# Kernel tuning notes

Hardware: AMD Instinct MI355X
Metric: run time of the kernel (lower is better)

The kernel has to match this reference:

```python
import jax, jax.numpy as jnp
import numpy as np

B, S, HID, LAYERS, HEADS, WINDOW = 2, 4096, 768, 4, 12, 256
W = WINDOW // 2            # one-sided window: each token attends to W left, W right
HD = HID // HEADS          # head dim = 64
MAXPOS = (S // WINDOW + 1) * WINDOW + 1
EPS = 1e-12                # Longformer layer_norm_eps


def layer_norm(x, g, b):
    m = x.mean(-1, keepdims=True)
    v = ((x - m) ** 2).mean(-1, keepdims=True)
    return (x - m) * jax.lax.rsqrt(v + EPS) * g + b


def sliding_window_attention(q, k, v, key_mask):
    # q,k,v: [B,H,S,D]; key_mask: [B,S] bool. Band attention: |i-j| <= W.
    Bz, Hh, Sl, D = q.shape
    nC = Sl // W
    q = q / jnp.sqrt(jnp.asarray(D, q.dtype))
    cidx = jnp.arange(nC)[:, None] + jnp.arange(3)[None, :]            # [nC,3] chunk gather
    kp = jnp.pad(k, ((0, 0), (0, 0), (W, W), (0, 0))).reshape(Bz, Hh, nC + 2, W, D)
    vp = jnp.pad(v, ((0, 0), (0, 0), (W, W), (0, 0))).reshape(Bz, Hh, nC + 2, W, D)
    kw = kp[:, :, cidx].reshape(Bz, Hh, nC, 3 * W, D)                  # keys for each query chunk
    vw = vp[:, :, cidx].reshape(Bz, Hh, nC, 3 * W, D)
    qc = q.reshape(Bz, Hh, nC, W, D)
    scores = jnp.einsum('bhcqd,bhckd->bhcqk', qc, kw)                  # [B,H,nC,W,3W]
    p = jnp.arange(W)[:, None]
    j = jnp.arange(3 * W)[None, :]
    band = (j >= p) & (j <= p + 2 * W)                                  # [W,3W] banded validity
    keypos = jnp.arange(nC)[:, None, None] * W + j[None] - W           # [nC,1,3W] global key idx
    inrange = (keypos >= 0) & (keypos < Sl)
    kmw = jnp.pad(key_mask, ((0, 0), (W, W))).reshape(Bz, nC + 2, W)[:, cidx].reshape(Bz, nC, 3 * W)
    mask = (band[None] & inrange)[None, None] & kmw[:, None, :, None, :]
    scores = jnp.where(mask, scores, jnp.asarray(-1e9, scores.dtype))
    probs = jax.nn.softmax(scores, axis=-1)
    out = jnp.einsum('bhcqk,bhckd->bhcqd', probs, vw)
    return out.reshape(Bz, Hh, Sl, D)


def heads_split(x):
    return x.reshape(x.shape[0], x.shape[1], HEADS, HD).transpose(0, 2, 1, 3)


def heads_merge(x):
    return x.transpose(0, 2, 1, 3).reshape(x.shape[0], x.shape[2], HID)


def forward(embeddings, pos_emb, tok_emb, emb_ln_g, emb_ln_b, Wq, bq, Wk, bk, Wv, bv,
            Wo, bo, ln1_g, ln1_b, Wi, bi, Wf, bf, ln2_g, ln2_b, Wp, bp, attention_mask):
    Sl = embeddings.shape[1]
    # Longformer embeddings: inputs_embeds + absolute positions (padding_idx+1 .. ) + token type 0
    h = embeddings + pos_emb[1:Sl + 1][None] + tok_emb[0][None, None]
    h = layer_norm(h, emb_ln_g, emb_ln_b)
    km = attention_mask.astype(bool)
    for l in range(LAYERS):
        q = heads_split(h @ Wq[l] + bq[l])
        k = heads_split(h @ Wk[l] + bk[l])
        v = heads_split(h @ Wv[l] + bv[l])
        a = heads_merge(sliding_window_attention(q, k, v, km))
        h = layer_norm(h + (a @ Wo[l] + bo[l]), ln1_g[l], ln1_b[l])
        f = jax.nn.gelu(h @ Wi[l] + bi[l], approximate=False) @ Wf[l] + bf[l]
        h = layer_norm(h + f, ln2_g[l], ln2_b[l])
    return jax.nn.sigmoid((h @ Wp + bp).squeeze(-1))


def setup_inputs() -> dict:
    key = jax.random.key(0)
    ks = jax.random.split(key, 12)
    nrm = lambda k, sh: jax.random.normal(k, sh, jnp.float32) * 0.02
    return dict(
        embeddings=jax.random.normal(ks[0], (B, S, HID), jnp.float32),
        attention_mask=jnp.ones((B, S), jnp.int32),
        pos_emb=nrm(ks[1], (MAXPOS, HID)),
        tok_emb=nrm(ks[2], (2, HID)),
        emb_ln_g=jnp.ones((HID,), jnp.float32),
        emb_ln_b=jnp.zeros((HID,), jnp.float32),
        Wq=nrm(ks[3], (LAYERS, HID, HID)), bq=jnp.zeros((LAYERS, HID), jnp.float32),
        Wk=nrm(ks[4], (LAYERS, HID, HID)), bk=jnp.zeros((LAYERS, HID), jnp.float32),
        Wv=nrm(ks[5], (LAYERS, HID, HID)), bv=jnp.zeros((LAYERS, HID), jnp.float32),
        Wo=nrm(ks[6], (LAYERS, HID, HID)), bo=jnp.zeros((LAYERS, HID), jnp.float32),
        ln1_g=jnp.ones((LAYERS, HID), jnp.float32), ln1_b=jnp.zeros((LAYERS, HID), jnp.float32),
        Wi=nrm(ks[7], (LAYERS, HID, 4 * HID)), bi=jnp.zeros((LAYERS, 4 * HID), jnp.float32),
        Wf=nrm(ks[8], (LAYERS, 4 * HID, HID)), bf=jnp.zeros((LAYERS, HID), jnp.float32),
        ln2_g=jnp.ones((LAYERS, HID), jnp.float32), ln2_b=jnp.zeros((LAYERS, HID), jnp.float32),
        Wp=nrm(ks[9], (HID, 1)), bp=jnp.zeros((1,), jnp.float32),
    )


def reference(embeddings, attention_mask, pos_emb, tok_emb, emb_ln_g, emb_ln_b, Wq, bq, Wk, bk,
              Wv, bv, Wo, bo, ln1_g, ln1_b, Wi, bi, Wf, bf, ln2_g, ln2_b, Wp, bp):
    return forward(embeddings, pos_emb, tok_emb, emb_ln_g, emb_ln_b, Wq, bq, Wk, bk, Wv, bv,
                   Wo, bo, ln1_g, ln1_b, Wi, bi, Wf, bf, ln2_g, ln2_b, Wp, bp, attention_mask)
```

## Files before the change

### kernel.cpp

```cpp
#include <hip/hip_runtime.h>
#include <hip/hip_bf16.h>


typedef __bf16 bf16;
typedef bf16  bf16x8  __attribute__((ext_vector_type(8)));
typedef float floatx4 __attribute__((ext_vector_type(4)));

#define MFMA16(a, b, c) __builtin_amdgcn_mfma_f32_16x16x32_bf16((a), (b), (c), 0, 0, 0)

__device__ __forceinline__ void gld_lds16(const bf16* gp, bf16* lp) {
  __builtin_amdgcn_global_load_lds(
      (const __attribute__((address_space(1))) void*)gp,
      (__attribute__((address_space(3))) void*)lp, 16, 0, 0);
}

__device__ __forceinline__ float fast_rcp(float x) {
  return __builtin_amdgcn_rcpf(x);
}

__device__ __forceinline__ float gelu_tanh(float v) {
  float t = 0.7978845608028654f * (v + 0.044715f * v * v * v);
  float e = __expf(2.f * t);
  float th = 1.f - 2.f * fast_rcp(e + 1.f);
  return 0.5f * v * (1.f + th);
}

static constexpr size_t SZ_WTQKV = (size_t)4 * 2304 * 768 * 2;
static constexpr size_t SZ_WTO   = (size_t)4 * 768 * 768 * 2;
static constexpr size_t SZ_WTI   = (size_t)4 * 3072 * 768 * 2;
static constexpr size_t SZ_WTF   = (size_t)4 * 768 * 3072 * 2;
static constexpr size_t SZ_BQKV  = (size_t)4 * 2304 * 4;
static constexpr size_t SZ_H32   = (size_t)8192 * 768 * 4;
static constexpr size_t SZ_HBF   = (size_t)8192 * 768 * 2;
static constexpr size_t SZ_QKV   = (size_t)8192 * 2304 * 2;
static constexpr size_t SZ_ATTN  = (size_t)8192 * 768 * 2;
static constexpr size_t SZ_TMP   = (size_t)8192 * 768 * 4;

static constexpr size_t OFF_WTQKV = 0;
static constexpr size_t OFF_WTO   = OFF_WTQKV + SZ_WTQKV;
static constexpr size_t OFF_WTI   = OFF_WTO   + SZ_WTO;
static constexpr size_t OFF_WTF   = OFF_WTI   + SZ_WTI;
static constexpr size_t OFF_BQKV  = OFF_WTF   + SZ_WTF;
static constexpr size_t OFF_H32   = OFF_BQKV  + SZ_BQKV;
static constexpr size_t OFF_HBF   = OFF_H32   + SZ_H32;
static constexpr size_t OFF_QKV   = OFF_HBF   + SZ_HBF;
static constexpr size_t OFF_ATTN  = OFF_QKV   + SZ_QKV;
static constexpr size_t OFF_TMP   = OFF_ATTN  + SZ_ATTN;
static constexpr size_t OFF_FFN1  = OFF_TMP   + SZ_TMP;

__global__ __launch_bounds__(256) void transpose_cast(
    const float* __restrict__ src, bf16* __restrict__ dst,
    int K, int N, long sStride, long dStride) {
  __shared__ float tile[32][33];
  const int l = blockIdx.z;
  src += (long)l * sStride;
  dst += (long)l * dStride;
  const int n0 = blockIdx.x * 32, k0 = blockIdx.y * 32;
  const int tx = threadIdx.x, ty = threadIdx.y;
#pragma unroll
  for (int i = 0; i < 4; ++i)
    tile[ty + i * 8][tx] = src[(long)(k0 + ty + i * 8) * N + n0 + tx];
  __syncthreads();
#pragma unroll
  for (int i = 0; i < 4; ++i)
    dst[(long)(n0 + ty + i * 8) * K + k0 + tx] = (bf16)tile[tx][ty + i * 8];
}

__global__ void bias_concat(const float* __restrict__ bq, const float* __restrict__ bk,
                            const float* __restrict__ bv, float* __restrict__ bqkv) {
  int i = blockIdx.x * 256 + threadIdx.x;
  if (i >= 4 * 2304) return;
  int l = i / 2304, p = i % 2304;
  float v = (p < 768) ? bq[l * 768 + p]
          : (p < 1536) ? bk[l * 768 + p - 768] : bv[l * 768 + p - 1536];
  bqkv[i] = v;
}

__device__ __forceinline__ void block_stats(float s1, float s2, float* red,
                                            float& mean, float& inv) {
  const int lane = threadIdx.x & 63, wave = threadIdx.x >> 6;
#pragma unroll
  for (int off = 32; off > 0; off >>= 1) {
    s1 += __shfl_down(s1, off, 64);
    s2 += __shfl_down(s2, off, 64);
  }
  if (lane == 0) { red[wave] = s1; red[4 + wave] = s2; }
  __syncthreads();
  s1 = red[0] + red[1] + red[2] + red[3];
  s2 = red[4] + red[5] + red[6] + red[7];
  mean = s1 * (1.f / 768.f);
  float var = s2 * (1.f / 768.f) - mean * mean;
  inv = rsqrtf(var + 1e-12f);
}

__global__ __launch_bounds__(256) void embed_ln_kernel(
    const float* __restrict__ emb, const float* __restrict__ pos,
    const float* __restrict__ tok, const float* __restrict__ g,
    const float* __restrict__ bta, float* __restrict__ h32, bf16* __restrict__ hbf) {
  __shared__ float red[8];
  const long base = (long)blockIdx.x * 768;
  const int s = blockIdx.x & 4095;
  const int t = threadIdx.x;
  float x[3], s1 = 0.f, s2 = 0.f;
#pragma unroll
  for (int i = 0; i < 3; ++i) {
    int c = t + i * 256;
    float v = emb[base + c] + pos[(long)(s + 1) * 768 + c] + tok[c];
    x[i] = v; s1 += v; s2 += v * v;
  }
  float mean, inv;
  block_stats(s1, s2, red, mean, inv);
#pragma unroll
  for (int i = 0; i < 3; ++i) {
    int c = t + i * 256;
    float y = (x[i] - mean) * inv * g[c] + bta[c];
    h32[base + c] = y;
    hbf[base + c] = (bf16)y;
  }
}

__global__ __launch_bounds__(256) void add_ln_kernel(
    float* __restrict__ h32, const bf16* __restrict__ p0,
    const bf16* __restrict__ p1, const float* __restrict__ bias,
    const float* __restrict__ g, const float* __restrict__ bta,
    bf16* __restrict__ hbf) {
  __shared__ float red[8];
  const long base = (long)blockIdx.x * 768;
  const int t = threadIdx.x;
  float x[3], s1 = 0.f, s2 = 0.f;
#pragma unroll
  for (int i = 0; i < 3; ++i) {
    int c = t + i * 256;
    float v = h32[base + c] + (float)p0[base + c] + (float)p1[base + c] + bias[c];
    x[i] = v; s1 += v; s2 += v * v;
  }
  float mean, inv;
  block_stats(s1, s2, red, mean, inv);
#pragma unroll
  for (int i = 0; i < 3; ++i) {
    int c = t + i * 256;
    float y = (x[i] - mean) * inv * g[c] + bta[c];
    h32[base + c] = y;
    hbf[base + c] = (bf16)y;
  }
}

template <int MODE>
__global__ __launch_bounds__(256) void gemm_kernel(
    const bf16* __restrict__ A, const bf16* __restrict__ BT,
    const float* __restrict__ bias, void* __restrict__ C0, void* __restrict__ C1,
    int N, int ld, int ksize) {
  __shared__ bf16 As[128 * 64];
  __shared__ bf16 Bs[128 * 64];
  const int tid  = threadIdx.x;
  const int wave = tid >> 6, lane = tid & 63, l15 = lane & 15, quad = lane >> 4;
  const int wm = wave >> 1, wn = wave & 1;
  const long m0 = (long)blockIdx.x * 128;
  const int  n0 = blockIdx.y * 128;
  const int  k0 = blockIdx.z * ksize;

  floatx4 acc[4][4] = {};
  const bf16* Ag = A + m0 * ld + k0;
  const bf16* Bg = BT + (long)n0 * ld + k0;
  const int rowoff = tid >> 3;
  const int sc_sw = (tid & 7) ^ (rowoff & 7);
  const int fsw = l15 & 7;

  for (int kt = 0; kt < ksize; kt += 64) {
#pragma unroll
    for (int p = 0; p < 4; ++p) {
      const int row = p * 32 + rowoff;
      gld_lds16(Ag + (long)row * ld + kt + sc_sw * 8, As + p * 2048 + wave * 512);
      gld_lds16(Bg + (long)row * ld + kt + sc_sw * 8, Bs + p * 2048 + wave * 512);
    }
    __syncthreads();
#pragma unroll
    for (int kk = 0; kk < 2; ++kk) {
      const int ch = ((kk * 4 + quad) ^ fsw) * 8;
      bf16x8 af[4], bfr[4];
#pragma unroll
      for (int mt = 0; mt < 4; ++mt)
        af[mt] = *(const bf16x8*)&As[(wm * 64 + mt * 16 + l15) * 64 + ch];
#pragma unroll
      for (int nt = 0; nt < 4; ++nt)
        bfr[nt] = *(const bf16x8*)&Bs[(wn * 64 + nt * 16 + l15) * 64 + ch];
#pragma unroll
      for (int mt = 0; mt < 4; ++mt)
#pragma unroll
        for (int nt = 0; nt < 4; ++nt)
          acc[mt][nt] = MFMA16(af[mt], bfr[nt], acc[mt][nt]);
    }
    __syncthreads();
  }

  bf16* Cg = (bf16*)((MODE == 0 && blockIdx.z != 0) ? C1 : C0);
  bf16* Es = As + wave * 1152;
#pragma unroll
  for (int mt = 0; mt < 4; ++mt) {
#pragma unroll
    for (int nt = 0; nt < 4; ++nt) {
      const float bb = (MODE == 0) ? 0.f : bias[n0 + wn * 64 + nt * 16 + l15];
#pragma unroll
      for (int r = 0; r < 4; ++r) {
        float v = acc[mt][nt][r] + bb;
        if (MODE == 2) v = gelu_tanh(v);
        Es[(quad * 4 + r) * 72 + nt * 16 + l15] = (bf16)v;
      }
    }
#pragma unroll
    for (int p = 0; p < 2; ++p) {
      const int rr = p * 8 + (lane >> 3);
      const int cc = (lane & 7) * 8;
      bf16x8 vv = *(const bf16x8*)&Es[rr * 72 + cc];
      *(bf16x8*)&Cg[(m0 + wm * 64 + mt * 16 + rr) * N + n0 + wn * 64 + cc] = vv;
    }
  }
}

__global__ __launch_bounds__(256) void vtrans_kernel(
    const bf16* __restrict__ qkv, bf16* __restrict__ vt) {
  __shared__ bf16 tile[64 * 68];
  const int s0 = blockIdx.x * 64, h = blockIdx.y, b = blockIdx.z;
  const int tid = threadIdx.x;
  const bf16* src = qkv + (long)b * 4096 * 2304 + 1536 + h * 64;
#pragma unroll
  for (int p = 0; p < 2; ++p) {
    const int i = p * 256 + tid;
    const int r = i >> 3, c = i & 7;
    *(uint4*)&tile[r * 68 + c * 8] = *(const uint4*)&src[(long)(s0 + r) * 2304 + c * 8];
  }
  __syncthreads();
  bf16* dst = vt + ((long)(b * 12 + h)) * 64 * 4096;
#pragma unroll
  for (int p = 0; p < 2; ++p) {
    const int i = p * 256 + tid;
    const int d = i >> 3, cs = i & 7;
    bf16 vals[8];
#pragma unroll
    for (int u = 0; u < 8; ++u) vals[u] = tile[(cs * 8 + u) * 68 + d];
    *(uint4*)&dst[(long)d * 4096 + s0 + cs * 8] = *(const uint4*)vals;
  }
}

__global__ __launch_bounds__(256) void attn_kernel(
    const bf16* __restrict__ qkv, const bf16* __restrict__ vt,
    const int* __restrict__ amask, bf16* __restrict__ attn_out) {
  constexpr int S = 4096, HID3 = 2304;
  __shared__ bf16 Ss[64 * 328];
  __shared__ bf16 Ts[64 * 64];
  __shared__ float redm[64], reds[64];

  const int x = blockIdx.x, q0 = x * 64, h = blockIdx.y, b = blockIdx.z;
  const int tid = threadIdx.x, wave = tid >> 6, lane = tid & 63;
  const int l15 = lane & 15, quad = lane >> 4;
  const int rowoff = tid >> 3;
  const int sc_sw = (tid & 7) ^ (rowoff & 7);
  const int fsw = l15 & 7;
  const int t_lo = (x < 2) ? (2 - x) : 0;
  const int t_hi = (x > 61) ? (66 - x) : 5;

  const bf16* Qb = qkv + (long)b * S * HID3 + h * 64;
  const bf16* Kb = Qb + 768;
  const bf16* Vt_bh = vt + ((long)(b * 12 + h)) * 64 * 4096;

  bf16x8 qf[2];
  {
    const long qrow = q0 + wave * 16 + l15;
    qf[0] = *(const bf16x8*)&Qb[qrow * HID3 + quad * 8];
    qf[1] = *(const bf16x8*)&Qb[qrow * HID3 + 32 + quad * 8];
  }

  float mrow[4] = {-3e38f, -3e38f, -3e38f, -3e38f};

  for (int t = t_lo; t < t_hi; ++t) {
    const int j0 = (x - 2 + t) * 64;
    __syncthreads();
#pragma unroll
    for (int p = 0; p < 2; ++p) {
      const int key = p * 32 + rowoff;
      gld_lds16(Kb + (long)(j0 + key) * HID3 + sc_sw * 8, &Ts[p * 2048 + wave * 512]);
    }
    __syncthreads();
    floatx4 sacc[4] = {};
#pragma unroll
    for (int kk = 0; kk < 2; ++kk) {
      const int ch = ((kk * 4 + quad) ^ fsw) * 8;
#pragma unroll
      for (int nt = 0; nt < 4; ++nt) {
        bf16x8 kf = *(const bf16x8*)&Ts[(nt * 16 + l15) * 64 + ch];
        sacc[nt] = MFMA16(qf[kk], kf, sacc[nt]);
      }
    }
#pragma unroll
    for (int nt = 0; nt < 4; ++nt) {
      const int jj = t * 64 + nt * 16 + l15;
      const int j = j0 + nt * 16 + l15;
      const bool jv = (amask[b * S + j] != 0);
#pragma unroll
      for (int r = 0; r < 4; ++r) {
        const int qi = wave * 16 + quad * 4 + r;
        const bool ok = jv && (jj >= qi) && (jj <= qi + 256);
        const float sv = ok ? sacc[nt][r] * 0.125f : -1e9f;
        mrow[r] = fmaxf(mrow[r], sv);
        Ss[(wave * 16 + quad * 4 + r) * 328 + jj] = (bf16)sv;
      }
    }
  }
#pragma unroll
  for (int off = 1; off < 16; off <<= 1)
#pragma unroll
    for (int r = 0; r < 4; ++r)
      mrow[r] = fmaxf(mrow[r], __shfl_xor(mrow[r], off, 64));
  if (l15 == 0) {
#pragma unroll
    for (int r = 0; r < 4; ++r) redm[wave * 16 + quad * 4 + r] = mrow[r];
  }
  __syncthreads();

  {
    const int row = wave * 16 + l15;
    const float mx = redm[row];
    float sum = 0.f;
    for (int c = t_lo * 8 + quad; c < t_hi * 8; c += 4) {
      bf16x8 pv = *(const bf16x8*)&Ss[row * 328 + c * 8];
#pragma unroll
      for (int u = 0; u < 8; ++u) {
        const float p = __expf((float)pv[u] - mx);
        sum += p;
        pv[u] = (bf16)p;
      }
      *(bf16x8*)&Ss[row * 328 + c * 8] = pv;
    }
    sum += __shfl_xor(sum, 16, 64);
    sum += __shfl_xor(sum, 32, 64);
    if (quad == 0) reds[row] = sum;
  }
  __syncthreads();

  floatx4 oacc[4] = {};
  for (int t = t_lo; t < t_hi; ++t) {
    const int j0 = (x - 2 + t) * 64;
    __syncthreads();
#pragma unroll
    for (int p = 0; p < 2; ++p) {
      const int d = p * 32 + rowoff;
      gld_lds16(Vt_bh + (long)d * 4096 + j0 + sc_sw * 8, &Ts[p * 2048 + wave * 512]);
    }
    __syncthreads();
#pragma unroll
    for (int kk = 0; kk < 2; ++kk) {
      const int ko = kk * 32 + quad * 8;
      const int ch = ((kk * 4 + quad) ^ fsw) * 8;
      bf16x8 pf = *(const bf16x8*)&Ss[(wave * 16 + l15) * 328 + t * 64 + ko];
#pragma unroll
      for (int nt = 0; nt < 4; ++nt) {
        bf16x8 vf = *(const bf16x8*)&Ts[(nt * 16 + l15) * 64 + ch];
        oacc[nt] = MFMA16(pf, vf, oacc[nt]);
      }
    }
  }

  float inv[4];
#pragma unroll
  for (int r = 0; r < 4; ++r) inv[r] = fast_rcp(reds[wave * 16 + quad * 4 + r]);
  const long orow = (long)b * S + q0 + wave * 16 + quad * 4;
#pragma unroll
  for (int nt = 0; nt < 4; ++nt)
#pragma unroll
    for (int r = 0; r < 4; ++r)
      attn_out[(orow + r) * 768 + h * 64 + nt * 16 + l15] =
          (bf16)(oacc[nt][r] * inv[r]);
}

__global__ __launch_bounds__(256) void final_kernel(
    const float* __restrict__ h32, const float* __restrict__ Wp,
    const float* __restrict__ bp, float* __restrict__ out) {
  const int wave = threadIdx.x >> 6, lane = threadIdx.x & 63;
  const long tok = (long)blockIdx.x * 4 + wave;
  float s = 0.f;
#pragma unroll
  for (int i = 0; i < 12; ++i) {
    const int c = lane + i * 64;
    s += h32[tok * 768 + c] * Wp[c];
  }
#pragma unroll
  for (int off = 32; off > 0; off >>= 1) s += __shfl_down(s, off, 64);
  if (lane == 0) out[tok] = fast_rcp(1.f + __expf(-(s + bp[0])));
}

extern "C" void kernel_launch(void* const* d_in, const int* in_sizes, int n_in,
                              void* d_out, int out_size, void* d_ws, size_t ws_size,
                              hipStream_t stream) {
  const float* emb   = (const float*)d_in[0];
  const int*   amask = (const int*)d_in[1];
  const float* pos   = (const float*)d_in[2];
  const float* tok   = (const float*)d_in[3];
  const float* elng  = (const float*)d_in[4];
  const float* elnb  = (const float*)d_in[5];
  const float* Wq = (const float*)d_in[6];   const float* bq = (const float*)d_in[7];
  const float* Wk = (const float*)d_in[8];   const float* bk = (const float*)d_in[9];
  const float* Wv = (const float*)d_in[10];  const float* bv = (const float*)d_in[11];
  const float* Wo = (const float*)d_in[12];  const float* bo = (const float*)d_in[13];
  const float* ln1g = (const float*)d_in[14]; const float* ln1b = (const float*)d_in[15];
  const float* Wi = (const float*)d_in[16];  const float* bi = (const float*)d_in[17];
  const float* Wf = (const float*)d_in[18];  const float* bfb = (const float*)d_in[19];
  const float* ln2g = (const float*)d_in[20]; const float* ln2b = (const float*)d_in[21];
  const float* Wp = (const float*)d_in[22];  const float* bp = (const float*)d_in[23];
  float* out = (float*)d_out;

  char* ws = (char*)d_ws;
  bf16*  WTqkv = (bf16*)(ws + OFF_WTQKV);
  bf16*  WTo   = (bf16*)(ws + OFF_WTO);
  bf16*  WTi   = (bf16*)(ws + OFF_WTI);
  bf16*  WTf   = (bf16*)(ws + OFF_WTF);
  float* bqkv  = (float*)(ws + OFF_BQKV);
  float* h32   = (float*)(ws + OFF_H32);
  bf16*  hbf   = (bf16*)(ws + OFF_HBF);
  bf16*  qkvb  = (bf16*)(ws + OFF_QKV);
  bf16*  part1 = (bf16*)(ws + OFF_QKV);
  bf16*  attnb = (bf16*)(ws + OFF_ATTN);
  bf16*  part0 = (bf16*)(ws + OFF_TMP);
  bf16*  vtb   = (bf16*)(ws + OFF_TMP);
  bf16*  ffn1  = (bf16*)(ws + OFF_FFN1);

  const dim3 tb(32, 8, 1);
  transpose_cast<<<dim3(24, 24, 4), tb, 0, stream>>>(Wq, WTqkv,               768, 768,  (long)768 * 768,  (long)2304 * 768);
  transpose_cast<<<dim3(24, 24, 4), tb, 0, stream>>>(Wk, WTqkv + 768 * 768,   768, 768,  (long)768 * 768,  (long)2304 * 768);
  transpose_cast<<<dim3(24, 24, 4), tb, 0, stream>>>(Wv, WTqkv + 1536 * 768,  768, 768,  (long)768 * 768,  (long)2304 * 768);
  transpose_cast<<<dim3(24, 24, 4), tb, 0, stream>>>(Wo, WTo,                 768, 768,  (long)768 * 768,  (long)768 * 768);
  transpose_cast<<<dim3(96, 24, 4), tb, 0, stream>>>(Wi, WTi,                 768, 3072, (long)768 * 3072, (long)3072 * 768);
  transpose_cast<<<dim3(24, 96, 4), tb, 0, stream>>>(Wf, WTf,                 3072, 768, (long)3072 * 768, (long)768 * 3072);
  bias_concat<<<36, 256, 0, stream>>>(bq, bk, bv, bqkv);

  embed_ln_kernel<<<8192, 256, 0, stream>>>(emb, pos, tok, elng, elnb, h32, hbf);

  for (int l = 0; l < 4; ++l) {
    gemm_kernel<1><<<dim3(64, 18, 1), 256, 0, stream>>>(
        hbf, WTqkv + (size_t)l * 2304 * 768, bqkv + l * 2304, qkvb, nullptr, 2304, 768, 768);
    vtrans_kernel<<<dim3(64, 12, 2), 256, 0, stream>>>(qkvb, vtb);
    attn_kernel<<<dim3(64, 12, 2), 256, 0, stream>>>(qkvb, vtb, amask, attnb);
    gemm_kernel<0><<<dim3(64, 6, 2), 256, 0, stream>>>(
        attnb, WTo + (size_t)l * 768 * 768, nullptr, part0, part1, 768, 768, 384);
    add_ln_kernel<<<8192, 256, 0, stream>>>(h32, part0, part1, bo + l * 768,
                                            ln1g + l * 768, ln1b + l * 768, hbf);
    gemm_kernel<2><<<dim3(64, 24, 1), 256, 0, stream>>>(
        hbf, WTi + (size_t)l * 3072 * 768, bi + l * 3072, ffn1, nullptr, 3072, 768, 768);
    gemm_kernel<0><<<dim3(64, 6, 2), 256, 0, stream>>>(
        ffn1, WTf + (size_t)l * 768 * 3072, nullptr, part0, part1, 768, 3072, 1536);
    add_ln_kernel<<<8192, 256, 0, stream>>>(h32, part0, part1, bfb + l * 768,
                                            ln2g + l * 768, ln2b + l * 768, hbf);
  }

  final_kernel<<<2048, 256, 0, stream>>>(h32, Wp, bp, out);
}
```

Before: 1.165 ms.

## Replace GEMM with 256x256-tile, 8-wave, double-buffered pipelined kernel

Result: no change. 1.169 ms (+0.3%).

```diff
diff --git a/kernel.cpp b/kernel.cpp
--- a/kernel.cpp
+++ b/kernel.cpp
@@ -145,58 +145,130 @@
   }
 }
 
+
+#define BARR() __builtin_amdgcn_s_barrier()
+#define LGKM0() asm volatile("s_waitcnt lgkmcnt(0)" ::: "memory")
+#define VMC6() asm volatile("s_waitcnt vmcnt(6)" ::: "memory")
+#define VMC0() asm volatile("s_waitcnt vmcnt(0)" ::: "memory")
+
+#define STG_A(t, h, buf)                                                      \
+  do {                                                                        \
+    gld_lds16(Ab + (long)((h) * 64 + rowoff) * ld + (t) * 64,                 \
+              &lds[buf][0][(h) * 8192 + wave * 512]);                         \
+    gld_lds16(Ab + (long)(128 + (h) * 64 + rowoff) * ld + (t) * 64,           \
+              &lds[buf][0][(h) * 8192 + 4096 + wave * 512]);                  \
+  } while (0)
+
+#define STG_B(t, h, buf)                                                      \
+  do {                                                                        \
+    gld_lds16(Bb + (long)(bq0 + (h) * 32) * ld + (t) * 64,                    \
+              &lds[buf][1][(h) * 8192 + wave * 512]);                         \
+    gld_lds16(Bb + (long)(bq0 + 128 + (h) * 32) * ld + (t) * 64,              \
+              &lds[buf][1][(h) * 8192 + 4096 + wave * 512]);                  \
+  } while (0)
+
+#define LDA_F(buf, mh)                                                        \
+  _Pragma("unroll") for (int mf = 0; mf < 4; ++mf)                            \
+  _Pragma("unroll") for (int kk = 0; kk < 2; ++kk)                            \
+      af[mf][kk] = *(const bf16x8*)&lds[buf][0][(mh) * 8192 +                 \
+          (wm * 64 + mf * 16 + l15) * 64 + ((kk * 4 + quad) ^ fsw) * 8];
+
+#define LDB_F(buf, nh, dst)                                                   \
+  _Pragma("unroll") for (int nf = 0; nf < 2; ++nf)                            \
+  _Pragma("unroll") for (int kk = 0; kk < 2; ++kk)                            \
+      dst[nf][kk] = *(const bf16x8*)&lds[buf][1][(nh) * 8192 +                \
+          (wn * 32 + nf * 16 + l15) * 64 + ((kk * 4 + quad) ^ fsw) * 8];
+
+#define MFMA_Q(mh, nh, B)                                                     \
+  do {                                                                        \
+    __builtin_amdgcn_s_setprio(1);                                            \
+    _Pragma("unroll") for (int kk = 0; kk < 2; ++kk)                          \
+    _Pragma("unroll") for (int mf = 0; mf < 4; ++mf)                          \
+    _Pragma("unroll") for (int nf = 0; nf < 2; ++nf)                          \
+        acc[(mh) * 4 + mf][(nh) * 2 + nf] = MFMA16(                           \
+            af[mf][kk], B[nf][kk], acc[(mh) * 4 + mf][(nh) * 2 + nf]);        \
+    __builtin_amdgcn_s_setprio(0);                                            \
+  } while (0)
+
 template <int MODE>
-__global__ __launch_bounds__(256) void gemm_kernel(
+__global__ __launch_bounds__(512, 2) void gemm256_kernel(
     const bf16* __restrict__ A, const bf16* __restrict__ BT,
     const float* __restrict__ bias, void* __restrict__ C0, void* __restrict__ C1,
     int N, int ld, int ksize) {
-  __shared__ bf16 As[128 * 64];
-  __shared__ bf16 Bs[128 * 64];
-  const int tid  = threadIdx.x;
+  __shared__ bf16 lds[2][2][16384];
+  const int tid = threadIdx.x;
   const int wave = tid >> 6, lane = tid & 63, l15 = lane & 15, quad = lane >> 4;
-  const int wm = wave >> 1, wn = wave & 1;
-  const long m0 = (long)blockIdx.x * 128;
-  const int  n0 = blockIdx.y * 128;
-  const int  k0 = blockIdx.z * ksize;
-
-  floatx4 acc[4][4] = {};
-  const bf16* Ag = A + m0 * ld + k0;
-  const bf16* Bg = BT + (long)n0 * ld + k0;
+  const int wm = wave >> 2, wn = wave & 3;
+  const long m0 = (long)blockIdx.x * 256;
+  const int n0 = blockIdx.y * 256;
+  const int k0 = blockIdx.z * ksize;
   const int rowoff = tid >> 3;
-  const int sc_sw = (tid & 7) ^ (rowoff & 7);
+  const int c_sw = (tid & 7) ^ (rowoff & 7);
   const int fsw = l15 & 7;
-
-  for (int kt = 0; kt < ksize; kt += 64) {
-#pragma unroll
-    for (int p = 0; p < 4; ++p) {
-      const int row = p * 32 + rowoff;
-      gld_lds16(Ag + (long)row * ld + kt + sc_sw * 8, As + p * 2048 + wave * 512);
-      gld_lds16(Bg + (long)row * ld + kt + sc_sw * 8, Bs + p * 2048 + wave * 512);
-    }
-    __syncthreads();
-#pragma unroll
-    for (int kk = 0; kk < 2; ++kk) {
-      const int ch = ((kk * 4 + quad) ^ fsw) * 8;
-      bf16x8 af[4], bfr[4];
-#pragma unroll
-      for (int mt = 0; mt < 4; ++mt)
-        af[mt] = *(const bf16x8*)&As[(wm * 64 + mt * 16 + l15) * 64 + ch];
-#pragma unroll
-      for (int nt = 0; nt < 4; ++nt)
-        bfr[nt] = *(const bf16x8*)&Bs[(wn * 64 + nt * 16 + l15) * 64 + ch];
-#pragma unroll
-      for (int mt = 0; mt < 4; ++mt)
-#pragma unroll
-        for (int nt = 0; nt < 4; ++nt)
-          acc[mt][nt] = MFMA16(af[mt], bfr[nt], acc[mt][nt]);
-    }
-    __syncthreads();
-  }
-
+  const int bq0 = (tid >> 8) * 64 + (rowoff & 31);
+  const int niter = ksize >> 7;
+
+  const bf16* Ab = A + m0 * ld + k0 + c_sw * 8;
+  const bf16* Bb = BT + (long)n0 * ld + k0 + c_sw * 8;
+
+  floatx4 acc[8][4] = {};
+  bf16x8 af[4][2], bl[2][2], bh[2][2];
+
+  STG_A(0, 0, 0); STG_B(0, 0, 0); STG_B(0, 1, 0); STG_A(0, 1, 0);
+  STG_A(1, 0, 1); STG_B(1, 0, 1); STG_B(1, 1, 1);
+  VMC6();
+  BARR();
+
+  for (int it = 0; it < niter; ++it) {
+    const int te = 2 * it, to = te + 1;
+    const bool last = (it == niter - 1);
+    LDA_F(0, 0); LDB_F(0, 0, bl);
+    STG_A(to, 1, 1);
+    BARR(); LGKM0();
+    MFMA_Q(0, 0, bl);
+    BARR();
+    LDB_F(0, 1, bh);
+    if (!last) STG_A(te + 2, 0, 0);
+    BARR(); LGKM0();
+    MFMA_Q(0, 1, bh);
+    BARR();
+    LDA_F(0, 1);
+    if (!last) STG_B(te + 2, 0, 0);
+    BARR(); LGKM0();
+    MFMA_Q(1, 1, bh);
+    BARR();
+    if (!last) STG_B(te + 2, 1, 0);
+    BARR();
+    MFMA_Q(1, 0, bl);
+    if (last) { VMC0(); } else { VMC6(); }
+    BARR();
+    LDA_F(1, 0); LDB_F(1, 0, bl);
+    if (!last) STG_A(te + 2, 1, 0);
+    BARR(); LGKM0();
+    MFMA_Q(0, 0, bl);
+    BARR();
+    LDB_F(1, 1, bh);
+    if (!last) STG_A(to + 2, 0, 1);
+    BARR(); LGKM0();
+    MFMA_Q(0, 1, bh);
+    BARR();
+    LDA_F(1, 1);
+    if (!last) STG_B(to + 2, 0, 1);
+    BARR(); LGKM0();
+    MFMA_Q(1, 1, bh);
+    BARR();
+    if (!last) STG_B(to + 2, 1, 1);
+    BARR();
+    MFMA_Q(1, 0, bl);
+    if (!last) VMC6();
+    BARR();
+  }
+
+  __syncthreads();
   bf16* Cg = (bf16*)((MODE == 0 && blockIdx.z != 0) ? C1 : C0);
-  bf16* Es = As + wave * 1152;
-#pragma unroll
-  for (int mt = 0; mt < 4; ++mt) {
+  bf16* Es = &lds[0][0][0] + wave * 1152;
+#pragma unroll
+  for (int mt = 0; mt < 8; ++mt) {
 #pragma unroll
     for (int nt = 0; nt < 4; ++nt) {
       const float bb = (MODE == 0) ? 0.f : bias[n0 + wn * 64 + nt * 16 + l15];
@@ -212,7 +284,7 @@
       const int rr = p * 8 + (lane >> 3);
       const int cc = (lane & 7) * 8;
       bf16x8 vv = *(const bf16x8*)&Es[rr * 72 + cc];
-      *(bf16x8*)&Cg[(m0 + wm * 64 + mt * 16 + rr) * N + n0 + wn * 64 + cc] = vv;
+      *(bf16x8*)&Cg[(m0 + wm * 128 + mt * 16 + rr) * N + n0 + wn * 64 + cc] = vv;
     }
   }
 }
@@ -435,17 +507,17 @@
   embed_ln_kernel<<<8192, 256, 0, stream>>>(emb, pos, tok, elng, elnb, h32, hbf);
 
   for (int l = 0; l < 4; ++l) {
-    gemm_kernel<1><<<dim3(64, 18, 1), 256, 0, stream>>>(
+    gemm256_kernel<1><<<dim3(32, 9, 1), 512, 0, stream>>>(
         hbf, WTqkv + (size_t)l * 2304 * 768, bqkv + l * 2304, qkvb, nullptr, 2304, 768, 768);
     vtrans_kernel<<<dim3(64, 12, 2), 256, 0, stream>>>(qkvb, vtb);
     attn_kernel<<<dim3(64, 12, 2), 256, 0, stream>>>(qkvb, vtb, amask, attnb);
-    gemm_kernel<0><<<dim3(64, 6, 2), 256, 0, stream>>>(
+    gemm256_kernel<0><<<dim3(32, 3, 2), 512, 0, stream>>>(
         attnb, WTo + (size_t)l * 768 * 768, nullptr, part0, part1, 768, 768, 384);
     add_ln_kernel<<<8192, 256, 0, stream>>>(h32, part0, part1, bo + l * 768,
                                             ln1g + l * 768, ln1b + l * 768, hbf);
-    gemm_kernel<2><<<dim3(64, 24, 1), 256, 0, stream>>>(
+    gemm256_kernel<2><<<dim3(32, 12, 1), 512, 0, stream>>>(
         hbf, WTi + (size_t)l * 3072 * 768, bi + l * 3072, ffn1, nullptr, 3072, 768, 768);
-    gemm_kernel<0><<<dim3(64, 6, 2), 256, 0, stream>>>(
+    gemm256_kernel<0><<<dim3(32, 3, 2), 512, 0, stream>>>(
         ffn1, WTf + (size_t)l * 768 * 3072, nullptr, part0, part1, 768, 3072, 1536);
     add_ln_kernel<<<8192, 256, 0, stream>>>(h32, part0, part1, bfb + l * 768,
                                             ln2g + l * 768, ln2b + l * 768, hbf);
```

## Use 8-wave GEMM blocks with templated dims and cheaper GELU epilogue

Applied to the files above, without the earlier changes.

New measurement: 1.146 ms. No clear change (-1.6%).

```diff
diff --git a/kernel.cpp b/kernel.cpp
--- a/kernel.cpp
+++ b/kernel.cpp
@@ -18,11 +18,11 @@
   return __builtin_amdgcn_rcpf(x);
 }
 
-__device__ __forceinline__ float gelu_tanh(float v) {
-  float t = 0.7978845608028654f * (v + 0.044715f * v * v * v);
-  float e = __expf(2.f * t);
-  float th = 1.f - 2.f * fast_rcp(e + 1.f);
-  return 0.5f * v * (1.f + th);
+__device__ __forceinline__ float gelu_fast(float v) {
+  float x2 = v * v;
+  float u = __builtin_fmaf(x2, -0.07135481f, -1.59576912f);
+  float e = __expf(v * u);
+  return v * fast_rcp(1.f + e);
 }
 
 static constexpr size_t SZ_WTQKV = (size_t)4 * 2304 * 768 * 2;
@@ -145,75 +145,83 @@
   }
 }
 
-template <int MODE>
-__global__ __launch_bounds__(256) void gemm_kernel(
+template <int MODE, int N, int LD>
+__global__ __launch_bounds__(512, 4) void gemm_kernel(
     const bf16* __restrict__ A, const bf16* __restrict__ BT,
     const float* __restrict__ bias, void* __restrict__ C0, void* __restrict__ C1,
-    int N, int ld, int ksize) {
-  __shared__ bf16 As[128 * 64];
-  __shared__ bf16 Bs[128 * 64];
+    int ksize) {
+  __shared__ bf16 smem[16384];
+  bf16* As = smem;
+  bf16* Bs = smem + 8192;
   const int tid  = threadIdx.x;
   const int wave = tid >> 6, lane = tid & 63, l15 = lane & 15, quad = lane >> 4;
-  const int wm = wave >> 1, wn = wave & 1;
+  const int wm = wave >> 2, wn = wave & 3;
   const long m0 = (long)blockIdx.x * 128;
   const int  n0 = blockIdx.y * 128;
   const int  k0 = blockIdx.z * ksize;
 
-  floatx4 acc[4][4] = {};
-  const bf16* Ag = A + m0 * ld + k0;
-  const bf16* Bg = BT + (long)n0 * ld + k0;
+  floatx4 acc[4][2] = {};
   const int rowoff = tid >> 3;
   const int sc_sw = (tid & 7) ^ (rowoff & 7);
   const int fsw = l15 & 7;
+  const bf16* Ag = A + m0 * LD + k0 + sc_sw * 8;
+  const bf16* Bg = BT + (long)n0 * LD + k0 + sc_sw * 8;
 
   for (int kt = 0; kt < ksize; kt += 64) {
 #pragma unroll
-    for (int p = 0; p < 4; ++p) {
-      const int row = p * 32 + rowoff;
-      gld_lds16(Ag + (long)row * ld + kt + sc_sw * 8, As + p * 2048 + wave * 512);
-      gld_lds16(Bg + (long)row * ld + kt + sc_sw * 8, Bs + p * 2048 + wave * 512);
+    for (int p = 0; p < 2; ++p) {
+      const int row = p * 64 + rowoff;
+      gld_lds16(Ag + (long)row * LD + kt, As + p * 4096 + wave * 512);
+      gld_lds16(Bg + (long)row * LD + kt, Bs + p * 4096 + wave * 512);
     }
     __syncthreads();
 #pragma unroll
     for (int kk = 0; kk < 2; ++kk) {
       const int ch = ((kk * 4 + quad) ^ fsw) * 8;
-      bf16x8 af[4], bfr[4];
+      bf16x8 af[4], bfr[2];
+#pragma unroll
+      for (int nt = 0; nt < 2; ++nt)
+        bfr[nt] = *(const bf16x8*)&Bs[(wn * 32 + nt * 16 + l15) * 64 + ch];
 #pragma unroll
       for (int mt = 0; mt < 4; ++mt)
         af[mt] = *(const bf16x8*)&As[(wm * 64 + mt * 16 + l15) * 64 + ch];
 #pragma unroll
-      for (int nt = 0; nt < 4; ++nt)
-        bfr[nt] = *(const bf16x8*)&Bs[(wn * 64 + nt * 16 + l15) * 64 + ch];
-#pragma unroll
       for (int mt = 0; mt < 4; ++mt)
 #pragma unroll
-        for (int nt = 0; nt < 4; ++nt)
+        for (int nt = 0; nt < 2; ++nt)
           acc[mt][nt] = MFMA16(af[mt], bfr[nt], acc[mt][nt]);
     }
     __syncthreads();
   }
 
   bf16* Cg = (bf16*)((MODE == 0 && blockIdx.z != 0) ? C1 : C0);
-  bf16* Es = As + wave * 1152;
-#pragma unroll
-  for (int mt = 0; mt < 4; ++mt) {
-#pragma unroll
-    for (int nt = 0; nt < 4; ++nt) {
-      const float bb = (MODE == 0) ? 0.f : bias[n0 + wn * 64 + nt * 16 + l15];
-#pragma unroll
-      for (int r = 0; r < 4; ++r) {
-        float v = acc[mt][nt][r] + bb;
-        if (MODE == 2) v = gelu_tanh(v);
-        Es[(quad * 4 + r) * 72 + nt * 16 + l15] = (bf16)v;
+#pragma unroll
+  for (int h = 0; h < 2; ++h) {
+    if (wm == h) {
+#pragma unroll
+      for (int mt = 0; mt < 4; ++mt)
+#pragma unroll
+        for (int nt = 0; nt < 2; ++nt) {
+          const float bb = (MODE == 0) ? 0.f : bias[n0 + wn * 32 + nt * 16 + l15];
+#pragma unroll
+          for (int r = 0; r < 4; ++r) {
+            float v = acc[mt][nt][r] + bb;
+            if (MODE == 2) v = gelu_fast(v);
+            smem[(mt * 16 + quad * 4 + r) * 136 + wn * 32 + nt * 16 + l15] = (bf16)v;
+          }
+        }
+    }
+    __syncthreads();
+    {
+      const int row = tid >> 3;
+#pragma unroll
+      for (int p = 0; p < 2; ++p) {
+        const int chunk = (tid & 7) + p * 8;
+        bf16x8 vv = *(const bf16x8*)&smem[row * 136 + chunk * 8];
+        *(bf16x8*)&Cg[(m0 + h * 64 + row) * N + n0 + chunk * 8] = vv;
       }
     }
-#pragma unroll
-    for (int p = 0; p < 2; ++p) {
-      const int rr = p * 8 + (lane >> 3);
-      const int cc = (lane & 7) * 8;
-      bf16x8 vv = *(const bf16x8*)&Es[rr * 72 + cc];
-      *(bf16x8*)&Cg[(m0 + wm * 64 + mt * 16 + rr) * N + n0 + wn * 64 + cc] = vv;
-    }
+    __syncthreads();
   }
 }
 
@@ -435,18 +443,18 @@
   embed_ln_kernel<<<8192, 256, 0, stream>>>(emb, pos, tok, elng, elnb, h32, hbf);
 
   for (int l = 0; l < 4; ++l) {
-    gemm_kernel<1><<<dim3(64, 18, 1), 256, 0, stream>>>(
-        hbf, WTqkv + (size_t)l * 2304 * 768, bqkv + l * 2304, qkvb, nullptr, 2304, 768, 768);
+    gemm_kernel<1, 2304, 768><<<dim3(64, 18, 1), 512, 0, stream>>>(
+        hbf, WTqkv + (size_t)l * 2304 * 768, bqkv + l * 2304, qkvb, nullptr, 768);
     vtrans_kernel<<<dim3(64, 12, 2), 256, 0, stream>>>(qkvb, vtb);
     attn_kernel<<<dim3(64, 12, 2), 256, 0, stream>>>(qkvb, vtb, amask, attnb);
-    gemm_kernel<0><<<dim3(64, 6, 2), 256, 0, stream>>>(
-        attnb, WTo + (size_t)l * 768 * 768, nullptr, part0, part1, 768, 768, 384);
+    gemm_kernel<0, 768, 768><<<dim3(64, 6, 2), 512, 0, stream>>>(
+        attnb, WTo + (size_t)l * 768 * 768, nullptr, part0, part1, 384);
     add_ln_kernel<<<8192, 256, 0, stream>>>(h32, part0, part1, bo + l * 768,
                                             ln1g + l * 768, ln1b + l * 768, hbf);
-    gemm_kernel<2><<<dim3(64, 24, 1), 256, 0, stream>>>(
-        hbf, WTi + (size_t)l * 3072 * 768, bi + l * 3072, ffn1, nullptr, 3072, 768, 768);
-    gemm_kernel<0><<<dim3(64, 6, 2), 256, 0, stream>>>(
-        ffn1, WTf + (size_t)l * 768 * 3072, nullptr, part0, part1, 768, 3072, 1536);
+    gemm_kernel<2, 3072, 768><<<dim3(64, 24, 1), 512, 0, stream>>>(
+        hbf, WTi + (size_t)l * 3072 * 768, bi + l * 3072, ffn1, nullptr, 768);
+    gemm_kernel<0, 768, 3072><<<dim3(64, 6, 2), 512, 0, stream>>>(
+        ffn1, WTf + (size_t)l * 768 * 3072, nullptr, part0, part1, 1536);
     add_ln_kernel<<<8192, 256, 0, stream>>>(h32, part0, part1, bfb + l * 768,
                                             ln2g + l * 768, ln2b + l * 768, hbf);
   }
```
